# Optimization experiments

Hardware: AMD Instinct MI355X
Metric: run time of the kernel (lower is better)

Reference implementation:

```python
import jax, jax.numpy as jnp
import numpy as np

B, N, NPOINT, NSAMPLE = 8, 4096, 1024, 32
IN_CH = 29
MLP = [64, 64, 128]
D_IN = IN_CH + 3  # 32
D_OUT = 128
EPS = 1e-5


def setup_inputs() -> dict:
    key = jax.random.key(0)
    ks = jax.random.split(key, 32)
    inp = {}
    inp["xyz"] = jax.random.normal(ks[0], (B, 3, N), jnp.float32)
    inp["points"] = jax.random.normal(ks[1], (B, IN_CH, N), jnp.float32)
    last = IN_CH + 3
    for i, oc in enumerate(MLP):
        inp[f"mlp_w{i}"] = jax.random.normal(ks[2 + i], (oc, last), jnp.float32) * np.sqrt(2.0 / last).astype(np.float32)
        inp[f"mlp_b{i}"] = jnp.zeros((oc,), jnp.float32)
        inp[f"mlp_g{i}"] = jnp.ones((oc,), jnp.float32)
        inp[f"mlp_be{i}"] = jnp.zeros((oc,), jnp.float32)
        last = oc
    inp["conv1_w"] = jax.random.normal(ks[10], (D_OUT // 2, 4), jnp.float32) * np.float32(np.sqrt(2.0 / 4))
    inp["conv1_b"] = jnp.zeros((D_OUT // 2,), jnp.float32)
    inp["bn1_g"] = jnp.ones((D_OUT // 2,), jnp.float32)
    inp["bn1_be"] = jnp.zeros((D_OUT // 2,), jnp.float32)
    inp["conv2_w"] = jax.random.normal(ks[11], (D_OUT // 2, D_IN), jnp.float32) * np.float32(np.sqrt(2.0 / D_IN))
    inp["conv2_b"] = jnp.zeros((D_OUT // 2,), jnp.float32)
    inp["bn2_g"] = jnp.ones((D_OUT // 2,), jnp.float32)
    inp["bn2_be"] = jnp.zeros((D_OUT // 2,), jnp.float32)
    return inp


def _conv1x1(x, w, b):
    # x: [B,Cin,ns,S], w: [Cout,Cin] -> [B,Cout,ns,S]
    return jnp.einsum("bcns,oc->bons", x, w) + b[None, :, None, None]


def _bn_relu(x, g, be):
    # training-mode BatchNorm2d: batch stats over (B, ns, S), biased variance
    m = jnp.mean(x, axis=(0, 2, 3), keepdims=True)
    v = jnp.var(x, axis=(0, 2, 3), keepdims=True)
    y = g[None, :, None, None] * (x - m) * jax.lax.rsqrt(v + EPS) + be[None, :, None, None]
    return jax.nn.relu(y)


def _fps(xyz):
    # xyz: [B,N,3] -> centroid indices [B,NPOINT]; deterministic start at index 0
    Bn, Nn, _ = xyz.shape

    def step(carry, _):
        dist, far = carry
        cen = jnp.take_along_axis(xyz, far[:, None, None], axis=1)  # [B,1,3]
        d = jnp.sum((xyz - cen) ** 2, axis=-1)                      # [B,N]
        dist = jnp.minimum(dist, d)
        new_far = jnp.argmax(dist, axis=-1).astype(jnp.int32)
        return (dist, new_far), far

    init = (jnp.full((Bn, Nn), 1e10, xyz.dtype), jnp.zeros((Bn,), jnp.int32))
    _, cents = jax.lax.scan(step, init, None, length=NPOINT)
    return cents.T  # [B,NPOINT]


def _forward(xyz, points, mlp_params, conv1_w, conv1_b, bn1_g, bn1_be,
             conv2_w, conv2_b, bn2_g, bn2_be):
    xyz_t = xyz.transpose(0, 2, 1)      # [B,N,3]
    pts_t = points.transpose(0, 2, 1)   # [B,N,C]
    xyz_sg = jax.lax.stop_gradient(xyz_t)

    ct_idx = _fps(xyz_sg)                                   # [B,S]
    bidx = jnp.arange(B)[:, None]
    ct_xyz = xyz_t[bidx, ct_idx]                            # [B,S,3]

    # kNN via squared distances (indices only -> stop_gradient)
    ct_sg = jax.lax.stop_gradient(ct_xyz)
    d2 = (jnp.sum(ct_sg ** 2, -1)[:, :, None]
          + jnp.sum(xyz_sg ** 2, -1)[:, None, :]
          - 2.0 * jnp.einsum("bsc,bnc->bsn", ct_sg, xyz_sg))  # [B,S,N]
    _, gidx = jax.lax.top_k(-d2, NSAMPLE)                     # [B,S,ns]

    bidx3 = jnp.arange(B)[:, None, None]
    grouped_xyz = xyz_t[bidx3, gidx]                          # [B,S,ns,3]
    ft_xyz = grouped_xyz - ct_xyz[:, :, None, :]              # [B,S,ns,3]
    ft_points = jnp.concatenate([ft_xyz, pts_t[bidx3, gidx]], axis=-1)  # [B,S,ns,3+C]
    ft = ft_points.transpose(0, 3, 2, 1)                      # [B,3+C,ns,S]

    # shared MLP (conv-bn-relu stack), then max over neighbors
    x = ft
    for (w, b, g, be) in mlp_params:
        x = _bn_relu(_conv1x1(x, w, b), g, be)
    new_points1 = jnp.max(x, axis=2)                          # [B,mlp[-1],S]

    # relative positional encoding branch
    ct_p = ct_xyz.transpose(0, 2, 1)                          # [B,3,S]
    grouped_p = grouped_xyz.transpose(0, 3, 2, 1)             # [B,3,ns,S]
    rel = grouped_p - ct_p[:, :, None, :]                     # [B,3,ns,S]
    rd = jnp.sqrt(jnp.maximum(jnp.sum(rel ** 2, axis=1, keepdims=True), 1e-12))
    new_xyz = _bn_relu(_conv1x1(jnp.concatenate([rel, rd], axis=1), conv1_w, conv1_b), bn1_g, bn1_be)
    new_pts = _bn_relu(_conv1x1(ft, conv2_w, conv2_b), bn2_g, bn2_be)

    f_concat = jnp.concatenate([new_xyz, new_pts], axis=1)    # [B,d_out,ns,S]
    new_points2 = jnp.concatenate([jnp.mean(f_concat, axis=2), jnp.max(f_concat, axis=2)], axis=1)
    conv_points = jnp.concatenate([new_points1, new_points2], axis=1)  # [B,mlp[-1]+2*d_out,S]
    return ct_p, conv_points


def reference(xyz, points,
              mlp_w0, mlp_b0, mlp_g0, mlp_be0,
              mlp_w1, mlp_b1, mlp_g1, mlp_be1,
              mlp_w2, mlp_b2, mlp_g2, mlp_be2,
              conv1_w, conv1_b, bn1_g, bn1_be,
              conv2_w, conv2_b, bn2_g, bn2_be):
    mlp_params = [(mlp_w0, mlp_b0, mlp_g0, mlp_be0),
                  (mlp_w1, mlp_b1, mlp_g1, mlp_be1),
                  (mlp_w2, mlp_b2, mlp_g2, mlp_be2)]
    return _forward(xyz, points, mlp_params, conv1_w, conv1_b, bn1_g, bn1_be,
                    conv2_w, conv2_b, bn2_g, bn2_be)
```

## Files before the change

### kernel.cpp

```cpp
#include <hip/hip_runtime.h>
#include <cfloat>
#include <math.h>

constexpr int B_ = 8, N_ = 4096, S_ = 1024, NS_ = 32;
constexpr int R_ = B_ * S_ * NS_;
constexpr float EPS_ = 1e-5f;

__device__ __forceinline__ void dpp_max_u64(unsigned& hi, unsigned& lo) {
#define STEP_(ctrl) { \
    unsigned h2 = (unsigned)__builtin_amdgcn_update_dpp((int)hi, (int)hi, ctrl, 0xf, 0xf, false); \
    unsigned l2 = (unsigned)__builtin_amdgcn_update_dpp((int)lo, (int)lo, ctrl, 0xf, 0xf, false); \
    if (h2 > hi || (h2 == hi && l2 > lo)) { hi = h2; lo = l2; } }
    STEP_(0x111) STEP_(0x112) STEP_(0x114) STEP_(0x118) STEP_(0x142) STEP_(0x143)
#undef STEP_
}
__device__ __forceinline__ void dpp_min_u64(unsigned& hi, unsigned& lo) {
#define STEP_(ctrl) { \
    unsigned h2 = (unsigned)__builtin_amdgcn_update_dpp((int)hi, (int)hi, ctrl, 0xf, 0xf, false); \
    unsigned l2 = (unsigned)__builtin_amdgcn_update_dpp((int)lo, (int)lo, ctrl, 0xf, 0xf, false); \
    if (h2 < hi || (h2 == hi && l2 < lo)) { hi = h2; lo = l2; } }
    STEP_(0x111) STEP_(0x112) STEP_(0x114) STEP_(0x118) STEP_(0x142) STEP_(0x143)
#undef STEP_
}
__device__ __forceinline__ float dpp_sum_f32(float x) {
#define ADD_(ctrl, rm) { \
    int t_ = __builtin_amdgcn_update_dpp(0, __float_as_int(x), ctrl, rm, 0xf, true); \
    x += __int_as_float(t_); }
    ADD_(0x111, 0xf) ADD_(0x112, 0xf) ADD_(0x114, 0xf) ADD_(0x118, 0xf)
    ADD_(0x142, 0xa) ADD_(0x143, 0xc)
#undef ADD_
    return x;
}

__global__ __launch_bounds__(512) void fps_kernel(const float* __restrict__ xyz,
                                                  int* __restrict__ ct_idx) {
    int b = blockIdx.x;
    const float* xb = xyz + (size_t)b * 3 * N_;
    int t = threadIdx.x;
    __shared__ float sx[N_], sy[N_], sz[N_];
    __shared__ unsigned long long sb[2][8];
    for (int i = t; i < N_; i += 512) {
        sx[i] = xb[i];
        sy[i] = xb[N_ + i];
        sz[i] = xb[2 * N_ + i];
    }
    float px[8], py[8], pz[8], dist[8];
    unsigned inv[8];
#pragma unroll
    for (int j = 0; j < 8; j++) {
        int n = j * 512 + t;
        px[j] = xb[n];
        py[j] = xb[N_ + n];
        pz[j] = xb[2 * N_ + n];
        dist[j] = 1e10f;
        inv[j] = ~(unsigned)n;
    }
    __syncthreads();
    float cx = sx[0], cy = sy[0], cz = sz[0];
    int far = 0;
    int w = t >> 6;
    for (int it = 0; it < S_; it++) {
        if (t == 0) ct_idx[b * S_ + it] = far;
        unsigned long long pk[8];
#pragma unroll
        for (int j = 0; j < 8; j++) {
            float dx = px[j] - cx, dy = py[j] - cy, dz = pz[j] - cz;
            float d = dx * dx;
            d = fmaf(dy, dy, d);
            d = fmaf(dz, dz, d);
            dist[j] = fminf(dist[j], d);
            pk[j] = ((unsigned long long)__float_as_uint(dist[j]) << 32) | inv[j];
        }
        unsigned long long m4a = pk[0] > pk[1] ? pk[0] : pk[1];
        unsigned long long m4b = pk[2] > pk[3] ? pk[2] : pk[3];
        unsigned long long m4c = pk[4] > pk[5] ? pk[4] : pk[5];
        unsigned long long m4d = pk[6] > pk[7] ? pk[6] : pk[7];
        unsigned long long m2a = m4a > m4b ? m4a : m4b;
        unsigned long long m2b = m4c > m4d ? m4c : m4d;
        unsigned long long best = m2a > m2b ? m2a : m2b;
        unsigned hi = (unsigned)(best >> 32), lo = (unsigned)best;
        dpp_max_u64(hi, lo);
        int p = it & 1;
        if ((t & 63) == 63) sb[p][w] = ((unsigned long long)hi << 32) | lo;
        __syncthreads();
        unsigned long long b0 = sb[p][0], b1 = sb[p][1], b2 = sb[p][2], b3 = sb[p][3];
        unsigned long long b4 = sb[p][4], b5 = sb[p][5], b6 = sb[p][6], b7 = sb[p][7];
        unsigned long long ma = b0 > b1 ? b0 : b1;
        unsigned long long mb = b2 > b3 ? b2 : b3;
        unsigned long long mc = b4 > b5 ? b4 : b5;
        unsigned long long md = b6 > b7 ? b6 : b7;
        unsigned long long me = ma > mb ? ma : mb;
        unsigned long long mf = mc > md ? mc : md;
        unsigned long long bw = me > mf ? me : mf;
        far = (int)(~(unsigned)(bw & 0xffffffffu));
        cx = sx[far]; cy = sy[far]; cz = sz[far];
    }
}

__global__ __launch_bounds__(256) void knn_kernel(const float* __restrict__ xyz,
                                                  const int* __restrict__ ct_idx,
                                                  int* __restrict__ gidx) {
    int bs = blockIdx.x;
    int b = bs >> 10;
    const float* xb = xyz + (size_t)b * 3 * N_;
    int ci = ct_idx[bs];
    float cx = xb[ci], cy = xb[N_ + ci], cz = xb[2 * N_ + ci];
    float cs = cx * cx + cy * cy + cz * cz;
    int t = threadIdx.x;
    unsigned long long pk[16];
#pragma unroll
    for (int j = 0; j < 16; j++) {
        int n = j * 256 + t;
        float x = xb[n], y = xb[N_ + n], z = xb[2 * N_ + n];
        float xn = x * x + y * y + z * z;
        float dot = cx * x + cy * y + cz * z;
        float val = cs + xn - 2.f * dot;
        unsigned vb = __float_as_uint(val);
        unsigned key = (vb & 0x80000000u) ? ~vb : (vb | 0x80000000u);
        pk[j] = ((unsigned long long)key << 32) | (unsigned)n;
    }
    __shared__ unsigned long long sw[2][4];
    int out_base = bs * NS_;
    int w = t >> 6;
    for (int iter = 0; iter < NS_; iter++) {
        unsigned long long m8[8], m4[4];
#pragma unroll
        for (int j = 0; j < 8; j++) m8[j] = pk[2 * j] < pk[2 * j + 1] ? pk[2 * j] : pk[2 * j + 1];
#pragma unroll
        for (int j = 0; j < 4; j++) m4[j] = m8[2 * j] < m8[2 * j + 1] ? m8[2 * j] : m8[2 * j + 1];
        unsigned long long ma = m4[0] < m4[1] ? m4[0] : m4[1];
        unsigned long long mb = m4[2] < m4[3] ? m4[2] : m4[3];
        unsigned long long best = ma < mb ? ma : mb;
        unsigned hi = (unsigned)(best >> 32), lo = (unsigned)best;
        dpp_min_u64(hi, lo);
        int p = iter & 1;
        if ((t & 63) == 63) sw[p][w] = ((unsigned long long)hi << 32) | lo;
        __syncthreads();
        unsigned long long b0 = sw[p][0], b1 = sw[p][1], b2 = sw[p][2], b3 = sw[p][3];
        unsigned long long wa = b0 < b1 ? b0 : b1;
        unsigned long long wb = b2 < b3 ? b2 : b3;
        unsigned long long bw = wa < wb ? wa : wb;
        int n = (int)(unsigned)(bw & 0xffffffffu);
        if (t == 0) gidx[out_base + iter] = n;
        if ((n & 255) == t) pk[n >> 8] = 0xFFFFFFFF00000000ull | (unsigned)n;
    }
}

__global__ __launch_bounds__(256) void ctp_kernel(const float* __restrict__ xyz,
                                                  const int* __restrict__ ct_idx,
                                                  float* __restrict__ out) {
    int i = blockIdx.x * 256 + threadIdx.x;
    if (i >= B_ * 3 * S_) return;
    int b = i / (3 * S_);
    int rem = i - b * 3 * S_;
    int c = rem >> 10;
    int s = rem & (S_ - 1);
    int ci = ct_idx[b * S_ + s];
    out[i] = xyz[(size_t)b * 3 * N_ + (size_t)c * N_ + ci];
}

__global__ __launch_bounds__(256) void gather_kernel(const float* __restrict__ xyz,
                                                     const float* __restrict__ pts,
                                                     const int* __restrict__ ct_idx,
                                                     const int* __restrict__ gidx,
                                                     float* __restrict__ ft) {
    int r = blockIdx.x * 256 + threadIdx.x;
    int b = r >> 15;
    int s = (r >> 5) & (S_ - 1);
    int g = gidx[r];
    int ci = ct_idx[b * S_ + s];
    const float* xb = xyz + (size_t)b * 3 * N_;
    float rx = xb[g] - xb[ci];
    float ry = xb[N_ + g] - xb[N_ + ci];
    float rz = xb[2 * N_ + g] - xb[2 * N_ + ci];
    ft[r] = rx;
    ft[(size_t)R_ + r] = ry;
    ft[(size_t)2 * R_ + r] = rz;
    float rd = sqrtf(fmaxf(rx * rx + ry * ry + rz * rz, 1e-12f));
    ft[(size_t)32 * R_ + r] = rd;
    const float* pb = pts + (size_t)b * 29 * N_;
#pragma unroll
    for (int c = 0; c < 29; c++) ft[(size_t)(3 + c) * R_ + r] = pb[(size_t)c * N_ + g];
}

template <int CIN, bool AFF>
__global__ __launch_bounds__(256) void convk(const float* __restrict__ xin,
                                             const float* __restrict__ W,
                                             const float* __restrict__ bias,
                                             const float* __restrict__ ab,
                                             float* __restrict__ out0,
                                             float* __restrict__ out1,
                                             float* __restrict__ partial) {
    __shared__ float Ws[CIN][64];
    __shared__ float bs_[64];
    __shared__ float as_[CIN], bbs[CIN];
    __shared__ float red[4][64][2];
    int oc0 = blockIdx.y * 64;
    for (int i = threadIdx.x; i < CIN * 64; i += 256) {
        int o = i & 63, c = i >> 6;
        Ws[c][o] = W[(size_t)(oc0 + o) * CIN + c];
    }
    if (threadIdx.x < 64) bs_[threadIdx.x] = bias[oc0 + threadIdx.x];
    if (AFF) {
        for (int i = threadIdx.x; i < CIN; i += 256) { as_[i] = ab[i]; bbs[i] = ab[CIN + i]; }
    }
    __syncthreads();
    size_t r0 = (size_t)blockIdx.x * 512 + threadIdx.x;
    float acc0[64], acc1[64];
#pragma unroll
    for (int o = 0; o < 64; o++) { acc0[o] = 0.f; acc1[o] = 0.f; }
    for (int c = 0; c < CIN; c++) {
        float x0 = xin[(size_t)c * R_ + r0];
        float x1 = xin[(size_t)c * R_ + r0 + 256];
        if (AFF) {
            float a = as_[c], bb = bbs[c];
            x0 = fmaxf(fmaf(a, x0, bb), 0.f);
            x1 = fmaxf(fmaf(a, x1, bb), 0.f);
        }
#pragma unroll
        for (int o = 0; o < 64; o++) {
            float w = Ws[c][o];
            acc0[o] = fmaf(x0, w, acc0[o]);
            acc1[o] = fmaf(x1, w, acc1[o]);
        }
    }
    float* outp = blockIdx.y ? out1 : out0;
    int wv = threadIdx.x >> 6;
#pragma unroll
    for (int o = 0; o < 64; o++) {
        float bv = bs_[o];
        float y0 = acc0[o] + bv;
        float y1 = acc1[o] + bv;
        outp[(size_t)o * R_ + r0] = y0;
        outp[(size_t)o * R_ + r0 + 256] = y1;
        float s = y0 + y1;
        float q = fmaf(y0, y0, y1 * y1);
        s = dpp_sum_f32(s);
        q = dpp_sum_f32(q);
        if ((threadIdx.x & 63) == 63) { red[wv][o][0] = s; red[wv][o][1] = q; }
    }
    __syncthreads();
    if (threadIdx.x < 64) {
        int o = threadIdx.x;
        float s = red[0][o][0] + red[1][o][0] + red[2][o][0] + red[3][o][0];
        float q = red[0][o][1] + red[1][o][1] + red[2][o][1] + red[3][o][1];
        partial[(size_t)(oc0 + o) * 1024 + blockIdx.x] = s;
        partial[(size_t)(oc0 + o) * 1024 + 512 + blockIdx.x] = q;
    }
}

__global__ __launch_bounds__(256) void conv1_kernel(const float* __restrict__ ft,
                                                    const float* __restrict__ W,
                                                    const float* __restrict__ bias,
                                                    float* __restrict__ out,
                                                    float* __restrict__ partial) {
    __shared__ float Ws[4][64];
    __shared__ float bs_[64];
    __shared__ float red[4][64][2];
    {
        int i = threadIdx.x;
        if (i < 256) { int o = i & 63, c = i >> 6; Ws[c][o] = W[o * 4 + c]; }
    }
    if (threadIdx.x < 64) bs_[threadIdx.x] = bias[threadIdx.x];
    __syncthreads();
    size_t r0 = (size_t)blockIdx.x * 512 + threadIdx.x;
    float acc0[64], acc1[64];
#pragma unroll
    for (int o = 0; o < 64; o++) { acc0[o] = 0.f; acc1[o] = 0.f; }
    const int chs[4] = {0, 1, 2, 32};
#pragma unroll
    for (int c = 0; c < 4; c++) {
        int ch = chs[c];
        float x0 = ft[(size_t)ch * R_ + r0];
        float x1 = ft[(size_t)ch * R_ + r0 + 256];
#pragma unroll
        for (int o = 0; o < 64; o++) {
            float w = Ws[c][o];
            acc0[o] = fmaf(x0, w, acc0[o]);
            acc1[o] = fmaf(x1, w, acc1[o]);
        }
    }
    int wv = threadIdx.x >> 6;
#pragma unroll
    for (int o = 0; o < 64; o++) {
        float bv = bs_[o];
        float y0 = acc0[o] + bv;
        float y1 = acc1[o] + bv;
        out[(size_t)o * R_ + r0] = y0;
        out[(size_t)o * R_ + r0 + 256] = y1;
        float s = y0 + y1;
        float q = fmaf(y0, y0, y1 * y1);
        s = dpp_sum_f32(s);
        q = dpp_sum_f32(q);
        if ((threadIdx.x & 63) == 63) { red[wv][o][0] = s; red[wv][o][1] = q; }
    }
    __syncthreads();
    if (threadIdx.x < 64) {
        int o = threadIdx.x;
        float s = red[0][o][0] + red[1][o][0] + red[2][o][0] + red[3][o][0];
        float q = red[0][o][1] + red[1][o][1] + red[2][o][1] + red[3][o][1];
        partial[(size_t)o * 1024 + blockIdx.x] = s;
        partial[(size_t)o * 1024 + 512 + blockIdx.x] = q;
    }
}

__global__ __launch_bounds__(64) void statsf(const float* __restrict__ partial,
                                             const float* __restrict__ g,
                                             const float* __restrict__ be,
                                             float* __restrict__ ab, int C) {
    int c = blockIdx.x, t = threadIdx.x;
    float s = 0.f, q = 0.f;
    for (int i = t; i < 512; i += 64) {
        s += partial[(size_t)c * 1024 + i];
        q += partial[(size_t)c * 1024 + 512 + i];
    }
    s = dpp_sum_f32(s);
    q = dpp_sum_f32(q);
    if (t == 63) {
        float inv = 1.0f / (float)R_;
        float mean = s * inv;
        float var = q * inv - mean * mean;
        float a = g[c] / sqrtf(var + EPS_);
        ab[c] = a;
        ab[C + c] = be[c] - mean * a;
    }
}

__global__ __launch_bounds__(128) void final_max(const float* __restrict__ yA,
                                                 const float* __restrict__ yC,
                                                 const float* __restrict__ ab,
                                                 float* __restrict__ out) {
    int bs = blockIdx.x;
    int c = threadIdx.x;
    const float* src = (c < 64 ? yA + (size_t)c * R_ : yC + (size_t)(c - 64) * R_) + (size_t)bs * NS_;
    float a = ab[c], bb = ab[128 + c];
    const float4* s4 = reinterpret_cast<const float4*>(src);
    float m = -FLT_MAX;
#pragma unroll
    for (int i = 0; i < 8; i++) {
        float4 v = s4[i];
        m = fmaxf(m, fmaxf(fmaf(a, v.x, bb), 0.f));
        m = fmaxf(m, fmaxf(fmaf(a, v.y, bb), 0.f));
        m = fmaxf(m, fmaxf(fmaf(a, v.z, bb), 0.f));
        m = fmaxf(m, fmaxf(fmaf(a, v.w, bb), 0.f));
    }
    int b = bs >> 10, s = bs & (S_ - 1);
    out[24576 + (size_t)b * 393216 + (size_t)c * 1024 + s] = m;
}

__global__ __launch_bounds__(128) void final_meanmax(const float* __restrict__ z1,
                                                     const float* __restrict__ z2,
                                                     const float* __restrict__ ab1,
                                                     const float* __restrict__ ab2,
                                                     float* __restrict__ out) {
    int bs = blockIdx.x;
    int c = threadIdx.x;
    const float* src;
    float a, bb;
    if (c < 64) { src = z1 + (size_t)c * R_; a = ab1[c]; bb = ab1[64 + c]; }
    else        { src = z2 + (size_t)(c - 64) * R_; a = ab2[c - 64]; bb = ab2[64 + (c - 64)]; }
    src += (size_t)bs * NS_;
    const float4* s4 = reinterpret_cast<const float4*>(src);
    float m = -FLT_MAX, sm = 0.f;
#pragma unroll
    for (int i = 0; i < 8; i++) {
        float4 v = s4[i];
        float t0 = fmaxf(fmaf(a, v.x, bb), 0.f); sm += t0; m = fmaxf(m, t0);
        float t1 = fmaxf(fmaf(a, v.y, bb), 0.f); sm += t1; m = fmaxf(m, t1);
        float t2 = fmaxf(fmaf(a, v.z, bb), 0.f); sm += t2; m = fmaxf(m, t2);
        float t3 = fmaxf(fmaf(a, v.w, bb), 0.f); sm += t3; m = fmaxf(m, t3);
    }
    int b = bs >> 10, s = bs & (S_ - 1);
    size_t ob = 24576 + (size_t)b * 393216;
    out[ob + (size_t)(128 + c) * 1024 + s] = sm * 0.03125f;
    out[ob + (size_t)(256 + c) * 1024 + s] = m;
}

extern "C" void kernel_launch(void* const* d_in, const int* in_sizes, int n_in,
                              void* d_out, int out_size, void* d_ws, size_t ws_size,
                              hipStream_t stream) {
    const float* xyz = (const float*)d_in[0];
    const float* pts = (const float*)d_in[1];
    const float* W0 = (const float*)d_in[2];  const float* b0 = (const float*)d_in[3];
    const float* g0 = (const float*)d_in[4];  const float* be0 = (const float*)d_in[5];
    const float* W1 = (const float*)d_in[6];  const float* b1 = (const float*)d_in[7];
    const float* g1 = (const float*)d_in[8];  const float* be1 = (const float*)d_in[9];
    const float* W2 = (const float*)d_in[10]; const float* b2 = (const float*)d_in[11];
    const float* g2 = (const float*)d_in[12]; const float* be2 = (const float*)d_in[13];
    const float* c1w = (const float*)d_in[14]; const float* c1b = (const float*)d_in[15];
    const float* bg1 = (const float*)d_in[16]; const float* bbe1 = (const float*)d_in[17];
    const float* c2w = (const float*)d_in[18]; const float* c2b = (const float*)d_in[19];
    const float* bg2 = (const float*)d_in[20]; const float* bbe2 = (const float*)d_in[21];
    float* out = (float*)d_out;

    int* ct_idx = (int*)d_ws;
    int* gidx = ct_idx + B_ * S_;
    float* fbase = (float*)d_ws;
    float* ft = fbase + 270336;
    float* A = ft + (size_t)33 * R_;
    float* Bb = A + (size_t)64 * R_;
    float* C = Bb + (size_t)64 * R_;
    float* partial = C + (size_t)64 * R_;
    float* ab0 = partial + 131072;
    float* ab1 = ab0 + 128;
    float* ab2 = ab1 + 128;
    float* abz1 = ab2 + 256;
    float* abz2 = abz1 + 128;

    fps_kernel<<<B_, 512, 0, stream>>>(xyz, ct_idx);
    knn_kernel<<<B_ * S_, 256, 0, stream>>>(xyz, ct_idx, gidx);
    ctp_kernel<<<(B_ * 3 * S_ + 255) / 256, 256, 0, stream>>>(xyz, ct_idx, out);
    gather_kernel<<<R_ / 256, 256, 0, stream>>>(xyz, pts, ct_idx, gidx, ft);

    convk<32, false><<<dim3(R_ / 512, 1), 256, 0, stream>>>(ft, W0, b0, nullptr, A, nullptr, partial);
    statsf<<<64, 64, 0, stream>>>(partial, g0, be0, ab0, 64);
    convk<64, true><<<dim3(R_ / 512, 1), 256, 0, stream>>>(A, W1, b1, ab0, Bb, nullptr, partial);
    statsf<<<64, 64, 0, stream>>>(partial, g1, be1, ab1, 64);
    convk<64, true><<<dim3(R_ / 512, 2), 256, 0, stream>>>(Bb, W2, b2, ab1, A, C, partial);
    statsf<<<128, 64, 0, stream>>>(partial, g2, be2, ab2, 128);
    final_max<<<B_ * S_, 128, 0, stream>>>(A, C, ab2, out);

    convk<32, false><<<dim3(R_ / 512, 1), 256, 0, stream>>>(ft, c2w, c2b, nullptr, Bb, nullptr, partial);
    statsf<<<64, 64, 0, stream>>>(partial, bg2, bbe2, abz2, 64);

    conv1_kernel<<<R_ / 512, 256, 0, stream>>>(ft, c1w, c1b, A, partial);
    statsf<<<64, 64, 0, stream>>>(partial, bg1, bbe1, abz1, 64);

    final_meanmax<<<B_ * S_, 128, 0, stream>>>(A, Bb, abz1, abz2, out);
}
```

Baseline: 1.559 ms.

## Restructure FPS argmax: 256 threads, float-key reduction, ballot-based index recovery

The farthest-point-sampling kernel now uses 256 threads with 16 contiguous points per thread instead of 512 threads with 8 strided points. The per-iteration argmax no longer packs distance and index into 64-bit keys. It reduces float distances with an index tree inside each thread, runs a 32-bit DPP max across the wavefront, then uses a ballot and readlane to recover the lowest matching lane and its index. This is meant to cut the 64-bit compare work and shrink the cross-wave shared-memory reduction from 8 waves to 4. In exchange each thread holds more registers and does more serial work per iteration, and ties are now broken by the first lane and first element found, so the choice of index among equal distances may differ from before.

```diff
diff --git a/kernel.cpp b/kernel.cpp
--- a/kernel.cpp
+++ b/kernel.cpp
@@ -6,13 +6,12 @@
 constexpr int R_ = B_ * S_ * NS_;
 constexpr float EPS_ = 1e-5f;
 
-__device__ __forceinline__ void dpp_max_u64(unsigned& hi, unsigned& lo) {
-#define STEP_(ctrl) { \
-    unsigned h2 = (unsigned)__builtin_amdgcn_update_dpp((int)hi, (int)hi, ctrl, 0xf, 0xf, false); \
-    unsigned l2 = (unsigned)__builtin_amdgcn_update_dpp((int)lo, (int)lo, ctrl, 0xf, 0xf, false); \
-    if (h2 > hi || (h2 == hi && l2 > lo)) { hi = h2; lo = l2; } }
+__device__ __forceinline__ unsigned dpp_red_umax(unsigned x) {
+    unsigned t;
+#define STEP_(ctrl) t = (unsigned)__builtin_amdgcn_update_dpp((int)x, (int)x, ctrl, 0xf, 0xf, false); x = x > t ? x : t;
     STEP_(0x111) STEP_(0x112) STEP_(0x114) STEP_(0x118) STEP_(0x142) STEP_(0x143)
 #undef STEP_
+    return x;
 }
 __device__ __forceinline__ void dpp_min_u64(unsigned& hi, unsigned& lo) {
 #define STEP_(ctrl) { \
@@ -32,28 +31,26 @@
     return x;
 }
 
-__global__ __launch_bounds__(512) void fps_kernel(const float* __restrict__ xyz,
+__global__ __launch_bounds__(256) void fps_kernel(const float* __restrict__ xyz,
                                                   int* __restrict__ ct_idx) {
     int b = blockIdx.x;
     const float* xb = xyz + (size_t)b * 3 * N_;
     int t = threadIdx.x;
     __shared__ float sx[N_], sy[N_], sz[N_];
-    __shared__ unsigned long long sb[2][8];
-    for (int i = t; i < N_; i += 512) {
+    __shared__ unsigned long long sb[2][4];
+    for (int i = t; i < N_; i += 256) {
         sx[i] = xb[i];
         sy[i] = xb[N_ + i];
         sz[i] = xb[2 * N_ + i];
     }
-    float px[8], py[8], pz[8], dist[8];
-    unsigned inv[8];
-#pragma unroll
-    for (int j = 0; j < 8; j++) {
-        int n = j * 512 + t;
+    float px[16], py[16], pz[16], dist[16];
+#pragma unroll
+    for (int j = 0; j < 16; j++) {
+        int n = t * 16 + j;
         px[j] = xb[n];
         py[j] = xb[N_ + n];
         pz[j] = xb[2 * N_ + n];
         dist[j] = 1e10f;
-        inv[j] = ~(unsigned)n;
     }
     __syncthreads();
     float cx = sx[0], cy = sy[0], cz = sz[0];
@@ -61,38 +58,52 @@
     int w = t >> 6;
     for (int it = 0; it < S_; it++) {
         if (t == 0) ct_idx[b * S_ + it] = far;
-        unsigned long long pk[8];
-#pragma unroll
-        for (int j = 0; j < 8; j++) {
+#pragma unroll
+        for (int j = 0; j < 16; j++) {
             float dx = px[j] - cx, dy = py[j] - cy, dz = pz[j] - cz;
             float d = dx * dx;
             d = fmaf(dy, dy, d);
             d = fmaf(dz, dz, d);
             dist[j] = fminf(dist[j], d);
-            pk[j] = ((unsigned long long)__float_as_uint(dist[j]) << 32) | inv[j];
-        }
-        unsigned long long m4a = pk[0] > pk[1] ? pk[0] : pk[1];
-        unsigned long long m4b = pk[2] > pk[3] ? pk[2] : pk[3];
-        unsigned long long m4c = pk[4] > pk[5] ? pk[4] : pk[5];
-        unsigned long long m4d = pk[6] > pk[7] ? pk[6] : pk[7];
-        unsigned long long m2a = m4a > m4b ? m4a : m4b;
-        unsigned long long m2b = m4c > m4d ? m4c : m4d;
-        unsigned long long best = m2a > m2b ? m2a : m2b;
-        unsigned hi = (unsigned)(best >> 32), lo = (unsigned)best;
-        dpp_max_u64(hi, lo);
+        }
+        float v8[8], v4[4], v2[2];
+        int j8[8], j4[4], j2[2];
+#pragma unroll
+        for (int j = 0; j < 8; j++) {
+            bool ge = dist[2 * j] >= dist[2 * j + 1];
+            v8[j] = ge ? dist[2 * j] : dist[2 * j + 1];
+            j8[j] = ge ? 2 * j : 2 * j + 1;
+        }
+#pragma unroll
+        for (int j = 0; j < 4; j++) {
+            bool ge = v8[2 * j] >= v8[2 * j + 1];
+            v4[j] = ge ? v8[2 * j] : v8[2 * j + 1];
+            j4[j] = ge ? j8[2 * j] : j8[2 * j + 1];
+        }
+#pragma unroll
+        for (int j = 0; j < 2; j++) {
+            bool ge = v4[2 * j] >= v4[2 * j + 1];
+            v2[j] = ge ? v4[2 * j] : v4[2 * j + 1];
+            j2[j] = ge ? j4[2 * j] : j4[2 * j + 1];
+        }
+        bool ge0 = v2[0] >= v2[1];
+        float lmax = ge0 ? v2[0] : v2[1];
+        int jbest = ge0 ? j2[0] : j2[1];
+        unsigned wm = (unsigned)__builtin_amdgcn_readlane(
+            (int)dpp_red_umax(__float_as_uint(lmax)), 63);
+        unsigned long long lanes = __ballot(__float_as_uint(lmax) == wm);
+        int l = __ffsll(lanes) - 1;
+        int js = __builtin_amdgcn_readlane(jbest, l);
+        unsigned n = (unsigned)(((w << 6) + l) * 16 + js);
         int p = it & 1;
-        if ((t & 63) == 63) sb[p][w] = ((unsigned long long)hi << 32) | lo;
+        if ((t & 63) == 0)
+            sb[p][w] = ((unsigned long long)wm << 32) | (unsigned)~n;
         __syncthreads();
         unsigned long long b0 = sb[p][0], b1 = sb[p][1], b2 = sb[p][2], b3 = sb[p][3];
-        unsigned long long b4 = sb[p][4], b5 = sb[p][5], b6 = sb[p][6], b7 = sb[p][7];
         unsigned long long ma = b0 > b1 ? b0 : b1;
         unsigned long long mb = b2 > b3 ? b2 : b3;
-        unsigned long long mc = b4 > b5 ? b4 : b5;
-        unsigned long long md = b6 > b7 ? b6 : b7;
-        unsigned long long me = ma > mb ? ma : mb;
-        unsigned long long mf = mc > md ? mc : md;
-        unsigned long long bw = me > mf ? me : mf;
-        far = (int)(~(unsigned)(bw & 0xffffffffu));
+        unsigned long long bw = ma > mb ? ma : mb;
+        far = (int)(~(unsigned)(bw & 0xffffffffu)) & (N_ - 1);
         cx = sx[far]; cy = sy[far]; cz = sz[far];
     }
 }
@@ -407,7 +418,7 @@
     float* abz1 = ab2 + 256;
     float* abz2 = abz1 + 128;
 
-    fps_kernel<<<B_, 512, 0, stream>>>(xyz, ct_idx);
+    fps_kernel<<<B_, 256, 0, stream>>>(xyz, ct_idx);
     knn_kernel<<<B_ * S_, 256, 0, stream>>>(xyz, ct_idx, gidx);
     ctp_kernel<<<(B_ * 3 * S_ + 255) / 256, 256, 0, stream>>>(xyz, ct_idx, out);
     gather_kernel<<<R_ / 256, 256, 0, stream>>>(xyz, pts, ct_idx, gidx, ft);
```

New measurement: 1.513 ms. 2.9% less time.
